# Optimization experiments

Measured on AMD Instinct MI355X. Metric: run time of the kernel, lower is better.

## Reference

```python
import jax, jax.numpy as jnp
import numpy as np

N = 30000
F_IN = 500
HID = 16
OUT = 3
E = 960000


def setup_inputs() -> dict:
    key = jax.random.key(0)
    ks = jax.random.split(key, 10)
    x = jax.random.normal(ks[0], (N, F_IN), dtype=jnp.float32)
    edge_index = jax.random.randint(ks[1], (2, E), 0, N, dtype=jnp.int32)
    # CNN params (torch Conv1d: weight [out, in, k], bias [out])
    s1 = 1.0 / np.sqrt(1 * 3)
    s2 = 1.0 / np.sqrt(HID * 3)
    conv1_w = jax.random.uniform(ks[2], (HID, 1, 3), jnp.float32, -s1, s1)
    conv1_b = jax.random.uniform(ks[3], (HID,), jnp.float32, -s1, s1)
    conv2_w = jax.random.uniform(ks[4], (HID, HID, 3), jnp.float32, -s2, s2)
    conv2_b = jax.random.uniform(ks[5], (HID,), jnp.float32, -s2, s2)
    # GCNConv params (glorot weight [in, out], zero bias)
    g1 = np.sqrt(6.0 / (HID + HID))
    g2 = np.sqrt(6.0 / (HID + OUT))
    gcn1_w = jax.random.uniform(ks[6], (HID, HID), jnp.float32, -g1, g1)
    gcn1_b = jnp.zeros((HID,), jnp.float32)
    gcn2_w = jax.random.uniform(ks[7], (HID, OUT), jnp.float32, -g2, g2)
    gcn2_b = jnp.zeros((OUT,), jnp.float32)
    return {"x": x, "conv1_w": conv1_w, "conv1_b": conv1_b,
            "conv2_w": conv2_w, "conv2_b": conv2_b,
            "gcn1_w": gcn1_w, "gcn1_b": gcn1_b,
            "gcn2_w": gcn2_w, "gcn2_b": gcn2_b,
            "edge_index": edge_index}


def _conv1d(x, w, b):
    # x: [N, C_in, L], w: [C_out, C_in, 3], padding=1
    y = jax.lax.conv_general_dilated(
        x, w, window_strides=(1,), padding=[(1, 1)],
        dimension_numbers=("NCH", "OIH", "NCH"))
    return y + b[None, :, None]


def _gcn_conv(x, w, b, src, dst, n):
    # x: [n, d_in] -> [n, d_out]; Kipf normalization with self-loops
    h = x @ w
    loop = jnp.arange(n, dtype=src.dtype)
    s = jnp.concatenate([src, loop])
    d = jnp.concatenate([dst, loop])
    deg = jax.ops.segment_sum(jnp.ones_like(d, dtype=h.dtype), d, num_segments=n)
    dinv = jnp.where(deg > 0, jax.lax.rsqrt(deg), 0.0)
    norm = dinv[s] * dinv[d]                      # [E+n]
    msg = h[s] * norm[:, None]                    # gather + scale
    return jax.ops.segment_sum(msg, d, num_segments=n) + b


def reference(x, conv1_w, conv1_b, conv2_w, conv2_b,
              gcn1_w, gcn1_b, gcn2_w, gcn2_b, edge_index):
    # CNN feature extractor over feature axis
    h = x[:, None, :]                             # [N, 1, F_IN]
    h = jax.nn.relu(_conv1d(h, conv1_w, conv1_b))  # [N, HID, F_IN]
    h = jax.nn.relu(_conv1d(h, conv2_w, conv2_b))  # [N, HID, F_IN]
    h = jnp.max(h, axis=2)                        # global max pool -> [N, HID]
    # GCN
    src, dst = edge_index[0], edge_index[1]
    n = h.shape[0]
    h = jax.nn.relu(_gcn_conv(h, gcn1_w, gcn1_b, src, dst, n))
    h = _gcn_conv(h, gcn2_w, gcn2_b, src, dst, n)  # [N, OUT]
    return jax.nn.log_softmax(h, axis=1)
```

## Files before the change

kernel.cpp:

```cpp
#include <hip/hip_runtime.h>
#include <hip/hip_bf16.h>

#define N_NODES 30000
#define F_INLEN 500
#define HID 16
#define OUTC 3
#define NEDGE 960000
#define YP 16
#define NBIN 938
#define HBLK 128
#define EPRH (NEDGE / HBLK)
#define ECAP 1536

typedef float  f32x4 __attribute__((ext_vector_type(4)));
typedef float  f32x2 __attribute__((ext_vector_type(2)));
typedef short  s16x8 __attribute__((ext_vector_type(8)));

static __device__ __forceinline__ unsigned short f2bf(float f) {
    unsigned int u = __float_as_uint(f);
    unsigned int r = (u + 0x7fffu + ((u >> 16) & 1u)) >> 16;
    return (unsigned short)r;
}
static __device__ __forceinline__ unsigned int pack_bf16x2(float v0, float v1) {
#if __has_builtin(__builtin_amdgcn_cvt_pk_bf16_f32)
    typedef __bf16 bf16x2_t __attribute__((ext_vector_type(2)));
    union { bf16x2_t v; unsigned int u; } cv;
    cv.v = __builtin_amdgcn_cvt_pk_bf16_f32(v0, v1);
    return cv.u;
#else
    return __builtin_amdgcn_perm(__float_as_uint(v1), __float_as_uint(v0), 0x07060302);
#endif
}

__global__ __launch_bounds__(256) void hist_kernel(
    const float* __restrict__ w2, short* __restrict__ bfragsG,
    const int* __restrict__ dst, int* __restrict__ degi, int* __restrict__ cntbase)
{
    const int tid = threadIdx.x;
    if (blockIdx.x == HBLK) {
        if (tid < 64) {
            const int n16 = tid & 15, q = tid >> 4;
#pragma unroll
            for (int j = 0; j < 8; j++) {
                {
                    const int c = q * 8 + j;
                    const int t = c >> 4, i = c & 15;
                    bfragsG[tid * 16 + j] = (short)f2bf(w2[n16 * 48 + i * 3 + t]);
                }
                {
                    const int c = 32 + q * 8 + j;
                    short v = 0;
                    if (c < 48) { const int t = c >> 4, i = c & 15; v = (short)f2bf(w2[n16 * 48 + i * 3 + t]); }
                    bfragsG[tid * 16 + 8 + j] = v;
                }
            }
        }
        return;
    }
    __shared__ int histH[NBIN];
    for (int i = tid; i < NBIN; i += 256) histH[i] = 0;
    __syncthreads();
    const int e0 = blockIdx.x * EPRH;
    for (int e = e0 + tid; e < e0 + EPRH; e += 256) {
        const int d = dst[e];
        atomicAdd(&histH[d >> 5], 1);
        atomicAdd(&degi[d], 1);
    }
    __syncthreads();
    for (int i = tid; i < NBIN; i += 256) cntbase[blockIdx.x * NBIN + i] = histH[i];
}

__global__ __launch_bounds__(256, 8) void conv_reorder(
    const float* __restrict__ x,
    const float* __restrict__ w1, const float* __restrict__ b1,
    const float* __restrict__ b2, const short* __restrict__ bfragsG,
    const int* __restrict__ src, const int* __restrict__ dst,
    const int* __restrict__ degi, const int* __restrict__ cntbase,
    int* __restrict__ packed, int* __restrict__ binstart,
    float* __restrict__ h0)
{
    __shared__ __align__(16) unsigned short yh[516 * YP];
    __shared__ __align__(16) float xp[502];
    __shared__ float red[64];

    const int tid = threadIdx.x;

    if (blockIdx.x < HBLK) {
        int* scA    = (int*)yh;
        int* scB    = scA + NBIN;
        int* totb   = scB + NBIN;
        int* cursor = totb + NBIN;
        const int blk = blockIdx.x;
        for (int bin = tid; bin < NBIN; bin += 256) {
            int tot = 0, psum = 0;
            for (int k = 0; k < HBLK; k++) {
                const int c = cntbase[k * NBIN + bin];
                tot += c;
                if (k < blk) psum += c;
            }
            scA[bin]    = tot;
            totb[bin]   = tot;
            cursor[bin] = psum;
        }
        __syncthreads();
        int* pA = scA; int* pB = scB;
        for (int off = 1; off < NBIN; off <<= 1) {
            for (int i = tid; i < NBIN; i += 256)
                pB[i] = pA[i] + ((i >= off) ? pA[i - off] : 0);
            __syncthreads();
            int* tp = pA; pA = pB; pB = tp;
        }
        for (int i = tid; i < NBIN; i += 256) {
            const int excl = pA[i] - totb[i];
            cursor[i] += excl;
            if (blk == 0) binstart[i] = excl;
        }
        if (blk == 0 && tid == 0) binstart[NBIN] = NEDGE;
        __syncthreads();
        const int e0 = blk * EPRH;
        for (int e = e0 + tid; e < e0 + EPRH; e += 256) {
            const int d = dst[e];
            const int pos = atomicAdd(&cursor[d >> 5], 1);
            packed[pos] = src[e] | (d << 15);
        }
        return;
    }

    const int node = blockIdx.x - HBLK;
    const int dgi  = degi[node];
    const int lane = tid & 63;
    const int wave = tid >> 6;
    const int n16  = lane & 15;
    const int q    = lane >> 4;

    if (tid == 0) { xp[0] = 0.f; xp[501] = 0.f; }
    if (tid < 125) {
        const float4 v = ((const float4*)(x + (long long)node * F_INLEN))[tid];
        xp[4 * tid + 1] = v.x; xp[4 * tid + 2] = v.y;
        xp[4 * tid + 3] = v.z; xp[4 * tid + 4] = v.w;
    }
    {
        const int ri = tid >> 4;
        const int row = (ri == 0) ? 0 : (500 + ri);
        yh[row * YP + (tid & 15)] = 0;
    }
    const s16x8* bfp = (const s16x8*)(bfragsG + lane * 16);
    const s16x8 bh0 = bfp[0], bh1 = bfp[1];

    f32x2 wt0[8], wt1[8], wt2[8], bbv[8];
#pragma unroll
    for (int cp = 0; cp < 8; cp++) {
        const int c0 = 2 * cp, c1 = 2 * cp + 1;
        wt0[cp] = (f32x2){w1[c0 * 3 + 0], w1[c1 * 3 + 0]};
        wt1[cp] = (f32x2){w1[c0 * 3 + 1], w1[c1 * 3 + 1]};
        wt2[cp] = (f32x2){w1[c0 * 3 + 2], w1[c1 * 3 + 2]};
        bbv[cp] = (f32x2){b1[c0], b1[c1]};
    }
    __syncthreads();

    for (int p = tid; p < 500; p += 256) {
        const float x0 = xp[p], x1 = xp[p + 1], x2 = xp[p + 2];
        const f32x2 xv0 = {x0, x0}, xv1 = {x1, x1}, xv2 = {x2, x2};
        const f32x2 zero = {0.f, 0.f};
        unsigned int hp[8];
#pragma unroll
        for (int cp = 0; cp < 8; cp++) {
            f32x2 a = __builtin_elementwise_fma(wt0[cp], xv0, bbv[cp]);
            a = __builtin_elementwise_fma(wt1[cp], xv1, a);
            a = __builtin_elementwise_fma(wt2[cp], xv2, a);
            a = __builtin_elementwise_max(a, zero);
            hp[cp] = pack_bf16x2(a[0], a[1]);
        }
        uint4* d = (uint4*)&yh[(p + 1) * YP];
        d[0] = make_uint4(hp[0], hp[1], hp[2], hp[3]);
        d[1] = make_uint4(hp[4], hp[5], hp[6], hp[7]);
    }
    __syncthreads();

    const unsigned short* ybase = yh + (n16 + (q >> 1)) * YP + (q & 1) * 8
                                     + wave * (8 * 16 * YP);
    f32x4 mxv = {-3.0e38f, -3.0e38f, -3.0e38f, -3.0e38f};
    f32x4 mxt = {-3.0e38f, -3.0e38f, -3.0e38f, -3.0e38f};
#pragma unroll
    for (int it = 0; it < 8; it++) {
        const s16x8 ah0 = *(const s16x8*)(ybase + it * (16 * YP));
        const s16x8 ah1 = *(const s16x8*)(ybase + it * (16 * YP) + 2 * YP);
        f32x4 acc = {0.f, 0.f, 0.f, 0.f};
        acc = __builtin_amdgcn_mfma_f32_16x16x32_bf16(ah0, bh0, acc, 0, 0, 0);
        acc = __builtin_amdgcn_mfma_f32_16x16x32_bf16(ah1, bh1, acc, 0, 0, 0);
        if (it < 7) mxv = __builtin_elementwise_max(mxv, acc);
        else        mxt = __builtin_elementwise_max(mxt, acc);
    }
    if (wave < 3 || q == 0) mxv = __builtin_elementwise_max(mxv, mxt);
    float m = fmaxf(fmaxf(mxv[0], mxv[1]), fmaxf(mxv[2], mxv[3]));
    m = fmaxf(m, __shfl_xor(m, 16));
    m = fmaxf(m, __shfl_xor(m, 32));
    if (lane < 16) red[wave * 16 + lane] = m;
    __syncthreads();
    if (tid < 16) {
        const float mm = fmaxf(fmaxf(red[tid], red[16 + tid]), fmaxf(red[32 + tid], red[48 + tid]));
        const float dv = rsqrtf((float)(dgi + 1));
        h0[node * HID + tid] = fmaxf(mm + b2[tid], 0.f) * dv;
    }
}

__global__ __launch_bounds__(256) void agg1_kernel(
    const int* __restrict__ binstart, int* __restrict__ packed,
    const float* __restrict__ h0,
    const float* __restrict__ W1, const float* __restrict__ b1g,
    const float* __restrict__ W2, float4* __restrict__ t2p4,
    int* __restrict__ binofs)
{
    __shared__ float w1s[256];
    __shared__ float w2s[48];
    __shared__ float b1s[16];
    __shared__ float accS[32 * 17];
    __shared__ int eL[ECAP];
    __shared__ int srt[ECAP];
    __shared__ int h32[32], ls32[32], lofs32[32];
    const int tid = threadIdx.x;
    const int blk = blockIdx.x;
    w1s[tid] = W1[tid];
    if (tid < 48) w2s[tid] = W2[tid];
    if (tid < 16) b1s[tid] = b1g[tid];
    if (tid < 32) h32[tid] = 0;
    const int beg = binstart[blk];
    const int cnt = binstart[blk + 1] - beg;
    __syncthreads();
    for (int j = tid; j < cnt; j += 256) {
        const int p = packed[beg + j];
        eL[j] = p;
        atomicAdd(&h32[(p >> 15) & 31], 1);
    }
    __syncthreads();
    if (tid < 32) {
        const int v = h32[tid];
        int inc = v;
#pragma unroll
        for (int off = 1; off < 32; off <<= 1) {
            const int y = __shfl_up(inc, off);
            if (tid >= off) inc += y;
        }
        ls32[tid] = inc - v;
        lofs32[tid] = inc - v;
    }
    __syncthreads();
    for (int j = tid; j < cnt; j += 256) {
        const int p = eL[j];
        const int pos = atomicAdd(&lofs32[(p >> 15) & 31], 1);
        srt[pos] = p;
    }
    __syncthreads();
    for (int j = tid; j < cnt; j += 256) packed[beg + j] = srt[j];
    if (tid < 32) {
        binofs[blk * 64 + tid]      = ls32[tid];
        binofs[blk * 64 + 32 + tid] = h32[tid];
    }
    const int n = tid >> 3;
    const int eslot = (tid >> 2) & 1;
    const int q = tid & 3;
    const int node = blk * 32 + n;
    const bool valid = node < N_NODES;
    f32x4 acc = {0.f, 0.f, 0.f, 0.f};
    if (valid) {
        const int s0 = ls32[n];
        const int s1 = s0 + h32[n];
        for (int i = s0 + eslot; i < s1; i += 2) {
            const int s = srt[i] & 32767;
            acc += *(const f32x4*)(h0 + s * HID + q * 4);
        }
    }
#pragma unroll
    for (int c = 0; c < 4; c++) acc[c] += __shfl_xor(acc[c], 4);
    if (valid && eslot == 0) {
        acc += *(const f32x4*)(h0 + node * HID + q * 4);
        accS[n * 17 + q * 4 + 0] = acc[0];
        accS[n * 17 + q * 4 + 1] = acc[1];
        accS[n * 17 + q * 4 + 2] = acc[2];
        accS[n * 17 + q * 4 + 3] = acc[3];
    }
    __syncthreads();
    if (tid < 128) {
        const int n2 = tid >> 2;
        const int node2 = blk * 32 + n2;
        if (node2 < N_NODES) {
            const float dv = rsqrtf((float)(h32[n2] + 1));
            const int q2 = tid & 3;
            float y0 = 0.f, y1 = 0.f, y2 = 0.f, y3 = 0.f;
#pragma unroll
            for (int i = 0; i < 16; i++) {
                const float a = accS[n2 * 17 + i];
                y0 = fmaf(a, w1s[i * 16 + q2 * 4 + 0], y0);
                y1 = fmaf(a, w1s[i * 16 + q2 * 4 + 1], y1);
                y2 = fmaf(a, w1s[i * 16 + q2 * 4 + 2], y2);
                y3 = fmaf(a, w1s[i * 16 + q2 * 4 + 3], y3);
            }
            float d0 = 0.f, d1 = 0.f, d2 = 0.f;
            const float yv[4] = {y0, y1, y2, y3};
#pragma unroll
            for (int j = 0; j < 4; j++) {
                const int o = q2 * 4 + j;
                const float h = fmaxf(b1s[o] + dv * yv[j], 0.f);
                d0 = fmaf(h, w2s[o * 3 + 0], d0);
                d1 = fmaf(h, w2s[o * 3 + 1], d1);
                d2 = fmaf(h, w2s[o * 3 + 2], d2);
            }
            d0 += __shfl_xor(d0, 1); d0 += __shfl_xor(d0, 2);
            d1 += __shfl_xor(d1, 1); d1 += __shfl_xor(d1, 2);
            d2 += __shfl_xor(d2, 1); d2 += __shfl_xor(d2, 2);
            if (q2 == 0) t2p4[node2] = make_float4(d0 * dv, d1 * dv, d2 * dv, dv);
        }
    }
}

__global__ __launch_bounds__(256) void agg2_kernel(
    const int* __restrict__ binstart, const int* __restrict__ packed,
    const float4* __restrict__ t2p4, const int* __restrict__ binofs,
    const float* __restrict__ b2g, float* __restrict__ out)
{
    __shared__ int eL[ECAP];
    __shared__ int ofs[64];
    const int tid = threadIdx.x;
    const int blk = blockIdx.x;
    const int beg = binstart[blk];
    const int cnt = binstart[blk + 1] - beg;
    if (tid < 64) ofs[tid] = binofs[blk * 64 + tid];
    for (int j = tid; j < cnt; j += 256) eL[j] = packed[beg + j];
    __syncthreads();
    const int n = tid >> 3;
    const int ln8 = tid & 7;
    const int node = blk * 32 + n;
    float a0 = 0.f, a1 = 0.f, a2 = 0.f;
    if (node < N_NODES) {
        const int s0 = ofs[n];
        const int s1 = s0 + ofs[32 + n];
        for (int i = s0 + ln8; i < s1; i += 8) {
            const int s = eL[i] & 32767;
            const float4 v = t2p4[s];
            a0 += v.x; a1 += v.y; a2 += v.z;
        }
    }
#pragma unroll
    for (int msk = 1; msk < 8; msk <<= 1) {
        a0 += __shfl_xor(a0, msk);
        a1 += __shfl_xor(a1, msk);
        a2 += __shfl_xor(a2, msk);
    }
    if (ln8 == 0 && node < N_NODES) {
        const float4 self = t2p4[node];
        const float dv = self.w;
        const float z0 = b2g[0] + dv * (a0 + self.x);
        const float z1 = b2g[1] + dv * (a1 + self.y);
        const float z2 = b2g[2] + dv * (a2 + self.z);
        const float m = fmaxf(z0, fmaxf(z1, z2));
        const float lg = m + logf(expf(z0 - m) + expf(z1 - m) + expf(z2 - m));
        out[node * 3 + 0] = z0 - lg;
        out[node * 3 + 1] = z1 - lg;
        out[node * 3 + 2] = z2 - lg;
    }
}

extern "C" void kernel_launch(void* const* d_in, const int* in_sizes, int n_in,
                              void* d_out, int out_size, void* d_ws, size_t ws_size,
                              hipStream_t stream)
{
    const float* x   = (const float*)d_in[0];
    const float* w1  = (const float*)d_in[1];
    const float* b1  = (const float*)d_in[2];
    const float* w2  = (const float*)d_in[3];
    const float* b2  = (const float*)d_in[4];
    const float* g1w = (const float*)d_in[5];
    const float* g1b = (const float*)d_in[6];
    const float* g2w = (const float*)d_in[7];
    const float* g2b = (const float*)d_in[8];
    const int*   ei  = (const int*)d_in[9];
    const int* src = ei;
    const int* dst = ei + NEDGE;

    float* ws = (float*)d_ws;
    float*  h0      = ws;
    float4* t2p4    = (float4*)(ws + 480000);
    int*    degi    = (int*)(ws + 600000);
    int*    cntbase = (int*)(ws + 630000);
    int*    binstart= (int*)(ws + 750064);
    int*    packed  = (int*)(ws + 751104);
    int*    binofs  = (int*)(ws + 1711104);
    short*  bfragsG = (short*)(ws + 1771136);
    float*  out     = (float*)d_out;

    hipMemsetAsync(degi, 0, N_NODES * sizeof(int), stream);
    hist_kernel<<<HBLK + 1, 256, 0, stream>>>(w2, bfragsG, dst, degi, cntbase);
    conv_reorder<<<HBLK + N_NODES, 256, 0, stream>>>(x, w1, b1, b2, bfragsG,
                                                     src, dst, degi, cntbase,
                                                     packed, binstart, h0);
    agg1_kernel<<<NBIN, 256, 0, stream>>>(binstart, packed, h0,
                                          g1w, g1b, g2w, t2p4, binofs);
    agg2_kernel<<<NBIN, 256, 0, stream>>>(binstart, packed, t2p4, binofs, g2b, out);
}
```

Baseline: 217.4 us.

## Process one node per wave in conv kernel, chunking conv1 rows through LDS

The fused conv kernel now assigns one node to each wave instead of one node per 256-thread block, so each block handles four nodes and the grid shrinks fourfold. Each wave computes conv1 rows in 48-row chunks into a private LDS slice and immediately consumes them with MFMA for conv2 plus max-pool. This removes all block-level barriers and the cross-wave reduction, and uses less LDS per block. In exchange each wave runs the chunk loop serially with some lanes idle, and the reorder blocks share the smaller LDS buffer.

```diff
diff --git a/kernel.cpp b/kernel.cpp
--- a/kernel.cpp
+++ b/kernel.cpp
@@ -11,6 +11,8 @@
 #define HBLK 128
 #define EPRH (NEDGE / HBLK)
 #define ECAP 1536
+#define WSLICE 3760
+#define XPOFF 2016
 
 typedef float  f32x4 __attribute__((ext_vector_type(4)));
 typedef float  f32x2 __attribute__((ext_vector_type(2)));
@@ -79,14 +81,12 @@
     int* __restrict__ packed, int* __restrict__ binstart,
     float* __restrict__ h0)
 {
-    __shared__ __align__(16) unsigned short yh[516 * YP];
-    __shared__ __align__(16) float xp[502];
-    __shared__ float red[64];
+    __shared__ __align__(16) unsigned char ldsb[4 * WSLICE];
 
     const int tid = threadIdx.x;
 
     if (blockIdx.x < HBLK) {
-        int* scA    = (int*)yh;
+        int* scA    = (int*)ldsb;
         int* scB    = scA + NBIN;
         int* totb   = scB + NBIN;
         int* cursor = totb + NBIN;
@@ -126,24 +126,31 @@
         return;
     }
 
-    const int node = blockIdx.x - HBLK;
-    const int dgi  = degi[node];
     const int lane = tid & 63;
     const int wave = tid >> 6;
     const int n16  = lane & 15;
     const int q    = lane >> 4;
-
-    if (tid == 0) { xp[0] = 0.f; xp[501] = 0.f; }
-    if (tid < 125) {
-        const float4 v = ((const float4*)(x + (long long)node * F_INLEN))[tid];
-        xp[4 * tid + 1] = v.x; xp[4 * tid + 2] = v.y;
-        xp[4 * tid + 3] = v.z; xp[4 * tid + 4] = v.w;
-    }
+    const int node = (blockIdx.x - HBLK) * 4 + wave;
+    const int dgi  = degi[node];
+
+    float*          xpw = (float*)(ldsb + wave * WSLICE);
+    unsigned short* yb  = (unsigned short*)(ldsb + wave * WSLICE + XPOFF);
+
     {
-        const int ri = tid >> 4;
-        const int row = (ri == 0) ? 0 : (500 + ri);
-        yh[row * YP + (tid & 15)] = 0;
-    }
+        const float4* xr = (const float4*)(x + (long long)node * F_INLEN);
+        const float4 v0 = xr[lane];
+        if (lane == 0) xpw[0] = 0.f;
+        if (lane < 3) xpw[501 + lane] = 0.f;
+        xpw[4 * lane + 1] = v0.x; xpw[4 * lane + 2] = v0.y;
+        xpw[4 * lane + 3] = v0.z; xpw[4 * lane + 4] = v0.w;
+        if (lane < 61) {
+            const float4 v1 = xr[64 + lane];
+            const int b = 4 * (64 + lane);
+            xpw[b + 1] = v1.x; xpw[b + 2] = v1.y;
+            xpw[b + 3] = v1.z; xpw[b + 4] = v1.w;
+        }
+    }
+
     const s16x8* bfp = (const s16x8*)(bfragsG + lane * 16);
     const s16x8 bh0 = bfp[0], bh1 = bfp[1];
 
@@ -156,51 +163,75 @@
         wt2[cp] = (f32x2){w1[c0 * 3 + 2], w1[c1 * 3 + 2]};
         bbv[cp] = (f32x2){b1[c0], b1[c1]};
     }
-    __syncthreads();
-
-    for (int p = tid; p < 500; p += 256) {
-        const float x0 = xp[p], x1 = xp[p + 1], x2 = xp[p + 2];
-        const f32x2 xv0 = {x0, x0}, xv1 = {x1, x1}, xv2 = {x2, x2};
-        const f32x2 zero = {0.f, 0.f};
-        unsigned int hp[8];
-#pragma unroll
-        for (int cp = 0; cp < 8; cp++) {
-            f32x2 a = __builtin_elementwise_fma(wt0[cp], xv0, bbv[cp]);
-            a = __builtin_elementwise_fma(wt1[cp], xv1, a);
-            a = __builtin_elementwise_fma(wt2[cp], xv2, a);
-            a = __builtin_elementwise_max(a, zero);
-            hp[cp] = pack_bf16x2(a[0], a[1]);
-        }
-        uint4* d = (uint4*)&yh[(p + 1) * YP];
-        d[0] = make_uint4(hp[0], hp[1], hp[2], hp[3]);
-        d[1] = make_uint4(hp[4], hp[5], hp[6], hp[7]);
-    }
-    __syncthreads();
-
-    const unsigned short* ybase = yh + (n16 + (q >> 1)) * YP + (q & 1) * 8
-                                     + wave * (8 * 16 * YP);
+
+    const unsigned short* ybase = yb + (n16 + (q >> 1)) * YP + (q & 1) * 8;
     f32x4 mxv = {-3.0e38f, -3.0e38f, -3.0e38f, -3.0e38f};
-    f32x4 mxt = {-3.0e38f, -3.0e38f, -3.0e38f, -3.0e38f};
-#pragma unroll
-    for (int it = 0; it < 8; it++) {
-        const s16x8 ah0 = *(const s16x8*)(ybase + it * (16 * YP));
-        const s16x8 ah1 = *(const s16x8*)(ybase + it * (16 * YP) + 2 * YP);
-        f32x4 acc = {0.f, 0.f, 0.f, 0.f};
-        acc = __builtin_amdgcn_mfma_f32_16x16x32_bf16(ah0, bh0, acc, 0, 0, 0);
-        acc = __builtin_amdgcn_mfma_f32_16x16x32_bf16(ah1, bh1, acc, 0, 0, 0);
-        if (it < 7) mxv = __builtin_elementwise_max(mxv, acc);
-        else        mxt = __builtin_elementwise_max(mxt, acc);
-    }
-    if (wave < 3 || q == 0) mxv = __builtin_elementwise_max(mxv, mxt);
+
+    auto conv_rows = [&](int c, int nact) {
+        const int r = c - 1 + lane;
+        if (lane < nact) {
+            uint4* drow = (uint4*)(yb + lane * YP);
+            if ((unsigned)r <= 499u) {
+                const float x0 = xpw[r], x1 = xpw[r + 1], x2 = xpw[r + 2];
+                const f32x2 xv0 = {x0, x0}, xv1 = {x1, x1}, xv2 = {x2, x2};
+                const f32x2 zero = {0.f, 0.f};
+                unsigned int hp[8];
+#pragma unroll
+                for (int cp = 0; cp < 8; cp++) {
+                    f32x2 a = __builtin_elementwise_fma(wt0[cp], xv0, bbv[cp]);
+                    a = __builtin_elementwise_fma(wt1[cp], xv1, a);
+                    a = __builtin_elementwise_fma(wt2[cp], xv2, a);
+                    a = __builtin_elementwise_max(a, zero);
+                    hp[cp] = pack_bf16x2(a[0], a[1]);
+                }
+                drow[0] = make_uint4(hp[0], hp[1], hp[2], hp[3]);
+                drow[1] = make_uint4(hp[4], hp[5], hp[6], hp[7]);
+            } else {
+                drow[0] = make_uint4(0u, 0u, 0u, 0u);
+                drow[1] = make_uint4(0u, 0u, 0u, 0u);
+            }
+        }
+    };
+
+#pragma unroll 1
+    for (int c = 0; c < 480; c += 48) {
+        conv_rows(c, 50);
+#pragma unroll
+        for (int t = 0; t < 3; t++) {
+            const s16x8 a0 = *(const s16x8*)(ybase + t * (16 * YP));
+            const s16x8 a1 = *(const s16x8*)(ybase + t * (16 * YP) + 2 * YP);
+            f32x4 acc = {0.f, 0.f, 0.f, 0.f};
+            acc = __builtin_amdgcn_mfma_f32_16x16x32_bf16(a0, bh0, acc, 0, 0, 0);
+            acc = __builtin_amdgcn_mfma_f32_16x16x32_bf16(a1, bh1, acc, 0, 0, 0);
+            mxv = __builtin_elementwise_max(mxv, acc);
+        }
+    }
+    {
+        conv_rows(480, 35);
+        {
+            const s16x8 a0 = *(const s16x8*)(ybase);
+            const s16x8 a1 = *(const s16x8*)(ybase + 2 * YP);
+            f32x4 acc = {0.f, 0.f, 0.f, 0.f};
+            acc = __builtin_amdgcn_mfma_f32_16x16x32_bf16(a0, bh0, acc, 0, 0, 0);
+            acc = __builtin_amdgcn_mfma_f32_16x16x32_bf16(a1, bh1, acc, 0, 0, 0);
+            mxv = __builtin_elementwise_max(mxv, acc);
+        }
+        {
+            const s16x8 a0 = *(const s16x8*)(ybase + 16 * YP);
+            const s16x8 a1 = *(const s16x8*)(ybase + 16 * YP + 2 * YP);
+            f32x4 acc = {0.f, 0.f, 0.f, 0.f};
+            acc = __builtin_amdgcn_mfma_f32_16x16x32_bf16(a0, bh0, acc, 0, 0, 0);
+            acc = __builtin_amdgcn_mfma_f32_16x16x32_bf16(a1, bh1, acc, 0, 0, 0);
+            if (q == 0) mxv = __builtin_elementwise_max(mxv, acc);
+        }
+    }
+
     float m = fmaxf(fmaxf(mxv[0], mxv[1]), fmaxf(mxv[2], mxv[3]));
     m = fmaxf(m, __shfl_xor(m, 16));
     m = fmaxf(m, __shfl_xor(m, 32));
-    if (lane < 16) red[wave * 16 + lane] = m;
-    __syncthreads();
-    if (tid < 16) {
-        const float mm = fmaxf(fmaxf(red[tid], red[16 + tid]), fmaxf(red[32 + tid], red[48 + tid]));
+    if (lane < 16) {
         const float dv = rsqrtf((float)(dgi + 1));
-        h0[node * HID + tid] = fmaxf(mm + b2[tid], 0.f) * dv;
+        h0[node * HID + lane] = fmaxf(m + b2[lane], 0.f) * dv;
     }
 }
 
@@ -390,9 +421,9 @@
 
     hipMemsetAsync(degi, 0, N_NODES * sizeof(int), stream);
     hist_kernel<<<HBLK + 1, 256, 0, stream>>>(w2, bfragsG, dst, degi, cntbase);
-    conv_reorder<<<HBLK + N_NODES, 256, 0, stream>>>(x, w1, b1, b2, bfragsG,
-                                                     src, dst, degi, cntbase,
-                                                     packed, binstart, h0);
+    conv_reorder<<<HBLK + (N_NODES / 4), 256, 0, stream>>>(x, w1, b1, b2, bfragsG,
+                                                           src, dst, degi, cntbase,
+                                                           packed, binstart, h0);
     agg1_kernel<<<NBIN, 256, 0, stream>>>(binstart, packed, h0,
                                           g1w, g1b, g2w, t2p4, binofs);
     agg2_kernel<<<NBIN, 256, 0, stream>>>(binstart, packed, t2p4, binofs, g2b, out);
```

Result: slower. 255.3 us (+17.4%).
